# Performance work log

Hardware: AMD Instinct MI355X
Metric: run time of the kernel (lower is better)

## Reference

```python
import jax, jax.numpy as jnp
import numpy as np

B, F, H, W = 1, 4, 20, 44
P = H * W            # 880 tokens per frame (20*44, from max_attention_size = 15*880)
S = F * P            # 3520 packed tokens
DIM, NH, FFN, OUT = 1536, 12, 6144, 64   # OUT = prod(patch_size)*out_dim = 4*16
HD = DIM // NH       # 128
C = HD // 2          # 64 rotary complex pairs
EPS = 1e-6


def _rope_angles():
    # Wan 3D RoPE: split C pairs as (C-2*(C//3), C//3, C//3) over (frame, h, w)
    cf, ch, cw = C - 2 * (C // 3), C // 3, C // 3
    def tab(n, cp):
        inv = 1.0 / (10000.0 ** (np.arange(cp) / cp))
        return np.outer(np.arange(n), inv)
    af = np.broadcast_to(tab(F, cf)[:, None, None, :], (F, H, W, cf))
    ah = np.broadcast_to(tab(H, ch)[None, :, None, :], (F, H, W, ch))
    aw = np.broadcast_to(tab(W, cw)[None, None, :, :], (F, H, W, cw))
    return np.concatenate([af, ah, aw], -1).reshape(S, C).astype(np.float32)


def setup_inputs() -> dict:
    key = jax.random.key(0)
    ks = jax.random.split(key, 24)
    g = lambda i, shape, s=0.02: jax.random.normal(ks[i], shape, dtype=jnp.float32) * s
    inp = {
        'x': jax.random.normal(ks[0], (B, S, DIM), dtype=jnp.float32),
        'e': g(1, (B, F, 6, DIM), 1.0),
        'e_head': g(2, (B, F, 2, DIM), 1.0),
        'rope_angles': jnp.asarray(_rope_angles()),
        'mod_block': g(3, (1, 6, DIM), 1.0 / float(np.sqrt(DIM))),
        'mod_head': g(4, (1, 2, DIM), 1.0 / float(np.sqrt(DIM))),
        'Wq': g(5, (DIM, DIM)), 'bq': jnp.zeros((DIM,), jnp.float32),
        'Wk': g(6, (DIM, DIM)), 'bk': jnp.zeros((DIM,), jnp.float32),
        'Wv': g(7, (DIM, DIM)), 'bv': jnp.zeros((DIM,), jnp.float32),
        'Wo': g(8, (DIM, DIM)), 'bo': jnp.zeros((DIM,), jnp.float32),
        'wq_norm': jnp.ones((DIM,), jnp.float32),
        'wk_norm': jnp.ones((DIM,), jnp.float32),
        'W1': g(9, (DIM, FFN)), 'b1': jnp.zeros((FFN,), jnp.float32),
        'W2': g(10, (FFN, DIM)), 'b2': jnp.zeros((DIM,), jnp.float32),
        'Wh': g(11, (DIM, OUT)), 'bh': jnp.zeros((OUT,), jnp.float32),
    }
    return inp


def _ln(x):
    # WanLayerNorm without elementwise affine
    m = jnp.mean(x, axis=-1, keepdims=True)
    v = jnp.var(x, axis=-1, keepdims=True)
    return (x - m) * jax.lax.rsqrt(v + EPS)


def _rms(x, w):
    return x * jax.lax.rsqrt(jnp.mean(x * x, axis=-1, keepdims=True) + EPS) * w


def _rope(t, ang):
    # t: [B,S,NH,HD]; adjacent pairs form complex numbers (view_as_complex style)
    tr = t.reshape(B, S, NH, C, 2)
    cos = jnp.cos(ang)[None, :, None, :]
    sin = jnp.sin(ang)[None, :, None, :]
    t0, t1 = tr[..., 0], tr[..., 1]
    return jnp.stack([t0 * cos - t1 * sin, t0 * sin + t1 * cos], -1).reshape(B, S, NH, HD)


def reference(x, e, e_head, rope_angles, mod_block, mod_head,
              Wq, bq, Wk, bk, Wv, bv, Wo, bo, wq_norm, wk_norm,
              W1, b1, W2, b2, Wh, bh):
    # ---- AdaLN modulation split (6-way) ----
    em = mod_block[:, None] + e                      # [B,F,6,DIM]
    e0, e1, e2, e3, e4, e5 = [em[:, :, i][:, :, None, :] for i in range(6)]

    xf = x.reshape(B, F, P, DIM)
    h = (_ln(xf) * (1 + e1) + e0).reshape(B, S, DIM)

    # ---- QK-RMSNorm + RoPE self attention (block-causal, block = one frame) ----
    q = _rope(_rms(h @ Wq + bq, wq_norm).reshape(B, S, NH, HD), rope_angles)
    k = _rope(_rms(h @ Wk + bk, wk_norm).reshape(B, S, NH, HD), rope_angles)
    v = (h @ Wv + bv).reshape(B, S, NH, HD)

    blk = jnp.arange(S) // P
    mask = blk[None, :] <= blk[:, None]              # [S,S] block-causal
    scores = jnp.einsum('bqhd,bkhd->bhqk', q, k) / np.float32(np.sqrt(HD))
    scores = jnp.where(mask[None, None], scores, jnp.float32(-1e30))
    attn = jax.nn.softmax(scores, axis=-1)
    y = jnp.einsum('bhqk,bkhd->bqhd', attn, v).reshape(B, S, DIM) @ Wo + bo

    xf = xf + y.reshape(B, F, P, DIM) * e2

    # ---- FFN with AdaLN modulation ----
    hf = (_ln(xf) * (1 + e4) + e3).reshape(B, S, DIM)
    ff = jax.nn.gelu(hf @ W1 + b1) @ W2 + b2
    xf = xf + ff.reshape(B, F, P, DIM) * e5

    # ---- OutputHead: modulated norm + linear ----
    eh = mod_head[:, None] + e_head                  # [B,F,2,DIM]
    eh0 = eh[:, :, 0][:, :, None, :]
    eh1 = eh[:, :, 1][:, :, None, :]
    out = (_ln(xf) * (1 + eh1) + eh0) @ Wh + bh      # [B,F,P,OUT]
    return out
```

## Files before the change

### kernel.cpp

```cpp
#include <hip/hip_runtime.h>
#include <cstdint>
#include <cstddef>

typedef __bf16 bf16;
typedef __bf16 bf16x2 __attribute__((ext_vector_type(2)));
typedef __bf16 bf16x8 __attribute__((ext_vector_type(8)));
typedef float f32x4 __attribute__((ext_vector_type(4)));
typedef unsigned int u32x4 __attribute__((ext_vector_type(4)));

#define S_TOK 3520
#define S_PAD 3584
#define P_TOK 880
#define NFRM 4
#define DIM 1536
#define NH 12
#define HD 128
#define FFN_D 6144
#define NOUT 64
#define EPSV 1e-6f
#define QSCALE 0.12751743f

__device__ __forceinline__ f32x4 mfma16(bf16x8 a, bf16x8 b, f32x4 c) {
  return __builtin_amdgcn_mfma_f32_16x16x32_bf16(a, b, c, 0, 0, 0);
}

__device__ __forceinline__ void gload_lds16(const bf16* g, bf16* l) {
  __builtin_amdgcn_global_load_lds(
      (const __attribute__((address_space(1))) unsigned int*)g,
      (__attribute__((address_space(3))) unsigned int*)l, 16, 0, 0);
}

__device__ __forceinline__ uint32_t pk2(float lo, float hi) {
  bf16x2 t;
  t[0] = (bf16)lo;
  t[1] = (bf16)hi;
  return __builtin_bit_cast(uint32_t, t);
}

__global__ __launch_bounds__(256) void k_prep(const float* __restrict__ e,
                                              const float* __restrict__ e_head,
                                              const float* __restrict__ mod_block,
                                              const float* __restrict__ mod_head,
                                              float* __restrict__ em,
                                              float* __restrict__ ehm) {
  int i = blockIdx.x * 256 + threadIdx.x;
  if (i < NFRM * 6 * DIM) em[i] = mod_block[i % (6 * DIM)] + e[i];
  int j = i - NFRM * 6 * DIM;
  if (j >= 0 && j < NFRM * 2 * DIM) ehm[j] = mod_head[j % (2 * DIM)] + e_head[j];
}

__global__ __launch_bounds__(256) void k_zero_vpad(bf16* __restrict__ vc) {
  size_t base = ((size_t)blockIdx.x * 28 + 27) * 4096 + 2048 + (size_t)threadIdx.x * 8;
#pragma unroll
  for (int i = 0; i < 8; ++i) vc[base + i] = (bf16)0.f;
}

__global__ __launch_bounds__(256) void k_transpose(const float* __restrict__ W,
                                                   bf16* __restrict__ Wt, int K, int N) {
  __shared__ float tile[32][33];
  int n0 = blockIdx.x * 32, k0 = blockIdx.y * 32;
  int tx = threadIdx.x & 31, ty = threadIdx.x >> 5;
#pragma unroll
  for (int j = 0; j < 4; ++j) {
    int k = k0 + ty * 4 + j;
    float v = (n0 + tx < N) ? W[(size_t)k * N + n0 + tx] : 0.f;
    tile[ty * 4 + j][tx] = v;
  }
  __syncthreads();
#pragma unroll
  for (int j = 0; j < 4; ++j) {
    int n = n0 + ty * 4 + j;
    if (n < N) Wt[(size_t)n * K + k0 + tx] = (bf16)tile[tx][ty * 4 + j];
  }
}

__global__ __launch_bounds__(256) void k_adaln(const float* __restrict__ in,
                                               bf16* __restrict__ out,
                                               const float* __restrict__ e_shift,
                                               const float* __restrict__ e_scale,
                                               int fstride) {
  int tok = blockIdx.x;
  int t = threadIdx.x;
  bf16* orow = out + (size_t)tok * DIM;
  if (tok >= S_TOK) {
#pragma unroll
    for (int i = 0; i < 6; ++i) orow[t * 6 + i] = (bf16)0.f;
    return;
  }
  const float* xrow = in + (size_t)tok * DIM;
  float v[6];
  float s = 0.f, sq = 0.f;
#pragma unroll
  for (int i = 0; i < 6; ++i) {
    v[i] = xrow[t * 6 + i];
    s += v[i];
    sq += v[i] * v[i];
  }
  for (int off = 32; off; off >>= 1) {
    s += __shfl_down(s, off);
    sq += __shfl_down(sq, off);
  }
  __shared__ float red[8];
  int wv = t >> 6, lane = t & 63;
  if (lane == 0) { red[wv] = s; red[4 + wv] = sq; }
  __syncthreads();
  float ts = red[0] + red[1] + red[2] + red[3];
  float tq = red[4] + red[5] + red[6] + red[7];
  float mean = ts * (1.f / DIM);
  float var = tq * (1.f / DIM) - mean * mean;
  float rstd = rsqrtf(var + EPSV);
  int f = tok / P_TOK;
  const float* sh = e_shift + (size_t)f * fstride;
  const float* sc = e_scale + (size_t)f * fstride;
#pragma unroll
  for (int i = 0; i < 6; ++i) {
    int d = t * 6 + i;
    orow[d] = (bf16)((v[i] - mean) * rstd * (1.f + sc[d]) + sh[d]);
  }
}

__global__ __launch_bounds__(256) void k_qkv_post(const float* __restrict__ qkv,
                                                  const float* __restrict__ wqn,
                                                  const float* __restrict__ wkn,
                                                  const float* __restrict__ ang,
                                                  bf16* __restrict__ qb,
                                                  bf16* __restrict__ kb,
                                                  bf16* __restrict__ vc) {
  int s = blockIdx.x;
  int t = threadIdx.x;
  const float* row = qkv + (size_t)s * 3 * DIM;
  float qv[6], kv[6], vv[6];
  float sqq = 0.f, sqk = 0.f;
  int d0 = t * 6;
#pragma unroll
  for (int i = 0; i < 6; ++i) {
    int d = d0 + i;
    qv[i] = row[d];
    kv[i] = row[DIM + d];
    vv[i] = row[2 * DIM + d];
    sqq += qv[i] * qv[i];
    sqk += kv[i] * kv[i];
  }
  float a1 = sqq, a2 = sqk;
  for (int off = 32; off; off >>= 1) {
    a1 += __shfl_down(a1, off);
    a2 += __shfl_down(a2, off);
  }
  __shared__ float red[8];
  int wv = t >> 6, lane = t & 63;
  if (lane == 0) { red[wv] = a1; red[4 + wv] = a2; }
  __syncthreads();
  float tq = red[0] + red[1] + red[2] + red[3];
  float tk = red[4] + red[5] + red[6] + red[7];
  float rq = rsqrtf(tq * (1.f / DIM) + EPSV);
  float rk = rsqrtf(tk * (1.f / DIM) + EPSV);
#pragma unroll
  for (int p = 0; p < 3; ++p) {
    int d = d0 + p * 2;
    int h = d >> 7;
    int hd = d & 127;
    int c = hd >> 1;
    float a = ang[(size_t)s * 64 + c];
    float sa, ca;
    sincosf(a, &sa, &ca);
    float q0 = qv[p * 2] * rq * wqn[d], q1 = qv[p * 2 + 1] * rq * wqn[d + 1];
    float k0 = kv[p * 2] * rk * wkn[d], k1 = kv[p * 2 + 1] * rk * wkn[d + 1];
    size_t base = ((size_t)h * S_TOK + s) * HD + hd;
    qb[base]     = (bf16)((q0 * ca - q1 * sa) * QSCALE);
    qb[base + 1] = (bf16)((q0 * sa + q1 * ca) * QSCALE);
    kb[base]     = (bf16)(k0 * ca - k1 * sa);
    kb[base + 1] = (bf16)(k0 * sa + k1 * ca);
  }
  int f = s / P_TOK;
  int l = s - f * P_TOK;
  int lb = l >> 5, gg = (l >> 3) & 3, r = l & 7;
#pragma unroll
  for (int i = 0; i < 6; ++i) {
    int d = d0 + i;
    int h = d >> 7, hd = d & 127;
    vc[((((size_t)(h * NFRM + f)) * 28 + lb) * 512 + gg * 128 + hd) * 8 + r] = (bf16)vv[i];
  }
}

__global__ __launch_bounds__(320) void k_attn(const bf16* __restrict__ qb,
                                              const bf16* __restrict__ kb,
                                              const bf16* __restrict__ vc,
                                              float* __restrict__ parto,
                                              float* __restrict__ partml) {
  __shared__ __align__(16) bf16 Ks[2][512 * 8];
  __shared__ __align__(16) bf16 Vs[2][512 * 8];
  int h = blockIdx.x / 110;
  int p = blockIdx.x % 110;
  int f = (p < 11) ? 0 : (p < 33) ? 1 : (p < 66) ? 2 : 3;
  int cum = (f == 0) ? 0 : (f == 1) ? 11 : (f == 2) ? 33 : 66;
  int w = p - cum;
  int kc = w / 11;
  int qt = f * 11 + w % 11;
  int slot = blockIdx.x;
  int t = threadIdx.x;
  int wv = t >> 6, lane = t & 63;
  int r16 = lane & 15, g = lane >> 4;
  int q0 = qt * 80 + wv * 16;
  int kv0 = kc * P_TOK;
  const bf16* qbase = qb + ((size_t)h * S_TOK + q0 + r16) * HD + g * 8;
  bf16x8 qf[4];
#pragma unroll
  for (int kk = 0; kk < 4; ++kk) qf[kk] = *(const bf16x8*)(qbase + kk * 32);
  f32x4 acc[8] = {};
  float mrow = -1e30f, lrow = 0.f;
  int src01 = r16 + ((2 * g) & 3) * 16;
  int src23 = src01 + 16;
  bool glo = (g < 2);
  int sB = t + 256;
  int kr0 = t >> 4, kl0 = t & 15;
  int ks0 = (kl0 & 8) | ((kl0 ^ kr0) & 7);
  int kr1 = sB >> 4, kl1 = sB & 15;
  int ks1 = (kl1 & 8) | ((kl1 ^ kr1) & 7);
  const bf16* kh = kb + (size_t)h * S_TOK * HD;
  const bf16* vchunk = vc + ((size_t)(h * NFRM + kc)) * 28 * 4096;
#define STAGE_ATT(buf, jj)                                                  \
  do {                                                                      \
    int kvoj = (jj) * 32;                                                   \
    int gr0 = kv0 + kvoj + kr0; if (gr0 >= S_TOK) gr0 = 0;                  \
    int gr1 = kv0 + kvoj + kr1; if (gr1 >= S_TOK) gr1 = 0;                  \
    gload_lds16(kh + (size_t)gr0 * HD + ks0 * 8, Ks[buf] + t * 8);          \
    gload_lds16(kh + (size_t)gr1 * HD + ks1 * 8, Ks[buf] + sB * 8);         \
    gload_lds16(vchunk + (size_t)(jj) * 4096 + t * 8, Vs[buf] + t * 8);     \
    gload_lds16(vchunk + (size_t)(jj) * 4096 + sB * 8, Vs[buf] + sB * 8);   \
  } while (0)
  const int nsteps = (P_TOK + 31) >> 5;
  if (t < 256) STAGE_ATT(0, 0);
  int cur = 0;
  for (int j = 0; j < nsteps; ++j) {
    int kvo = j * 32;
    if (j + 1 < nsteps) {
      if (t < 256) STAGE_ATT(cur ^ 1, j + 1);
      asm volatile("s_waitcnt vmcnt(4)" ::: "memory");
    } else {
      asm volatile("s_waitcnt vmcnt(0)" ::: "memory");
    }
    __builtin_amdgcn_s_barrier();
    f32x4 st0 = {0.f, 0.f, 0.f, 0.f}, st1 = {0.f, 0.f, 0.f, 0.f};
#pragma unroll
    for (int kk = 0; kk < 4; ++kk) {
      int sl = g + 4 * kk;
      int ss = (sl & 8) | ((sl ^ r16) & 7);
      bf16x8 k0 = *(const bf16x8*)(Ks[cur] + (r16 * 16 + ss) * 8);
      bf16x8 k1 = *(const bf16x8*)(Ks[cur] + ((16 + r16) * 16 + ss) * 8);
      st0 = mfma16(k0, qf[kk], st0);
      st1 = mfma16(k1, qf[kk], st1);
    }
    float hm = (kvo + 16 >= P_TOK) ? -1e30f : 0.f;
    float a0[4], a1[4];
#pragma unroll
    for (int r = 0; r < 4; ++r) {
      a0[r] = st0[r];
      a1[r] = st1[r] + hm;
    }
    float tm = fmaxf(fmaxf(fmaxf(a0[0], a0[1]), fmaxf(a0[2], a0[3])),
                     fmaxf(fmaxf(a1[0], a1[1]), fmaxf(a1[2], a1[3])));
    tm = fmaxf(tm, __shfl_xor(tm, 16));
    tm = fmaxf(tm, __shfl_xor(tm, 32));
    float mn = fmaxf(mrow, tm);
    float p0[4], p1[4], ps = 0.f;
#pragma unroll
    for (int r = 0; r < 4; ++r) {
      p0[r] = exp2f(a0[r] - mn);
      p1[r] = exp2f(a1[r] - mn);
      ps += p0[r] + p1[r];
    }
    float scl = exp2f(mrow - mn);
    mrow = mn;
    lrow = lrow * scl + ps;
    uint32_t A0 = pk2(p0[0], p0[1]), A1 = pk2(p0[2], p0[3]);
    uint32_t B0 = pk2(p1[0], p1[1]), B1 = pk2(p1[2], p1[3]);
    uint32_t sA0 = __shfl(A0, src01), sA1 = __shfl(A1, src01);
    uint32_t sB0 = __shfl(B0, src01), sB1 = __shfl(B1, src01);
    uint32_t tA0 = __shfl(A0, src23), tA1 = __shfl(A1, src23);
    uint32_t tB0 = __shfl(B0, src23), tB1 = __shfl(B1, src23);
    u32x4 wds;
    wds[0] = glo ? sA0 : sB0;
    wds[1] = glo ? sA1 : sB1;
    wds[2] = glo ? tA0 : tB0;
    wds[3] = glo ? tA1 : tB1;
    bf16x8 pb = __builtin_bit_cast(bf16x8, wds);
#pragma unroll
    for (int hb = 0; hb < 8; ++hb) {
      acc[hb][0] *= scl;
      acc[hb][1] *= scl;
      acc[hb][2] *= scl;
      acc[hb][3] *= scl;
    }
    const bf16* vsl = Vs[cur] + (size_t)(g * 128 + r16) * 8;
#pragma unroll
    for (int hb = 0; hb < 8; ++hb) {
      bf16x8 vfr = *(const bf16x8*)(vsl + hb * 128);
      acc[hb] = mfma16(vfr, pb, acc[hb]);
    }
    asm volatile("" ::: "memory");
    __builtin_amdgcn_s_barrier();
    cur ^= 1;
  }
#undef STAGE_ATT
  lrow += __shfl_xor(lrow, 16);
  lrow += __shfl_xor(lrow, 32);
  float* obase = parto + (((size_t)slot * 5 + wv) * 8) * 256;
#pragma unroll
  for (int hb = 0; hb < 8; ++hb) {
    *(f32x4*)(obase + (hb * 64 + lane) * 4) = acc[hb];
  }
  if (g == 0) {
    float* mlb = partml + ((size_t)slot * 5 + wv) * 32;
    mlb[r16] = mrow;
    mlb[16 + r16] = lrow;
  }
}

__global__ __launch_bounds__(256) void k_att_reduce(const float* __restrict__ parto,
                                                    const float* __restrict__ partml,
                                                    bf16* __restrict__ attb) {
  int b = blockIdx.x;
  int h = b / 44, qt = b % 44;
  int f = qt / 11, j = qt % 11;
  int cum = (f == 0) ? 0 : (f == 1) ? 11 : (f == 2) ? 33 : 66;
  int t = threadIdx.x;
  int d = t & 127, half = t >> 7;
  int hb = d >> 4, g = (d >> 2) & 3, r = d & 3;
  int q0 = qt * 80;
  for (int it = 0; it < 40; ++it) {
    int qloc = it + 40 * half;
    int wv = qloc >> 4, r16 = qloc & 15;
    float m[4], l[4];
    float mt = -1e30f;
    for (int kc = 0; kc <= f; ++kc) {
      int slot = h * 110 + cum + kc * 11 + j;
      const float* mlb = partml + ((size_t)slot * 5 + wv) * 32;
      m[kc] = mlb[r16];
      l[kc] = mlb[16 + r16];
      mt = fmaxf(mt, m[kc]);
    }
    float lt = 0.f, o = 0.f;
    for (int kc = 0; kc <= f; ++kc) {
      int slot = h * 110 + cum + kc * 11 + j;
      float wgt = exp2f(m[kc] - mt);
      lt += l[kc] * wgt;
      o += parto[(((size_t)slot * 5 + wv) * 8 + hb) * 256 + (g * 16 + r16) * 4 + r] * wgt;
    }
    attb[(size_t)(q0 + qloc) * DIM + h * HD + d] = (bf16)(o / lt);
  }
}

struct GemmP {
  const bf16* A;
  const bf16* Bt;
  int K;
  int Mtiles;
  int Ntiles;
  int Mreal;
  int mode;
  const float* bias0;
  const float* bias1;
  const float* bias2;
  const float* res;
  const float* emod;
  int e_fstride;
  float* outf;
  bf16* outb;
  int ldo;
};

__global__ __launch_bounds__(512, 4) void k_gemm(GemmP p) {
  int nwg = p.Mtiles * p.Ntiles;
  int bid = blockIdx.x;
  int xq = nwg >> 3, xr = nwg & 7;
  int xcd = bid & 7, jj = bid >> 3;
  int wg = (xcd < xr ? xcd * (xq + 1) : xr * (xq + 1) + (xcd - xr) * xq) + jj;
  int bm = wg % p.Mtiles;
  int bn = wg / p.Mtiles;
  __shared__ __align__(16) bf16 Asl[2][128 * 64];
  __shared__ __align__(16) bf16 Bsl[2][128 * 64];
  int t = threadIdx.x, lane = t & 63, wv = t >> 6;
  int r16 = lane & 15, g = lane >> 4;
  int s7 = r16 & 7;
  int wr = wv >> 2, wc = wv & 3;
  f32x4 acc[4][2] = {};
  const bf16* Ag = p.A + (size_t)bm * 128 * p.K;
  const bf16* Bg = p.Bt + (size_t)bn * 128 * p.K;
  int b0 = t, b1 = t + 512;
  int rw0 = b0 >> 3, cb0 = (b0 & 7) ^ (rw0 & 7);
  int rw1 = b1 >> 3, cb1 = (b1 & 7) ^ (rw1 & 7);
#define STAGE(d, kt)                                                          \
  do {                                                                        \
    int k0s = (kt) * 64;                                                      \
    gload_lds16(Ag + (size_t)rw0 * p.K + k0s + cb0 * 8, Asl[d] + b0 * 8);     \
    gload_lds16(Ag + (size_t)rw1 * p.K + k0s + cb1 * 8, Asl[d] + b1 * 8);     \
    gload_lds16(Bg + (size_t)rw0 * p.K + k0s + cb0 * 8, Bsl[d] + b0 * 8);     \
    gload_lds16(Bg + (size_t)rw1 * p.K + k0s + cb1 * 8, Bsl[d] + b1 * 8);     \
  } while (0)
  const int nt = p.K >> 6;
  STAGE(0, 0);
  int cur = 0;
  for (int tt = 0; tt < nt; ++tt) {
    if (tt + 1 < nt) {
      STAGE(cur ^ 1, tt + 1);
      asm volatile("s_waitcnt vmcnt(4)" ::: "memory");
    } else {
      asm volatile("s_waitcnt vmcnt(0)" ::: "memory");
    }
    __builtin_amdgcn_s_barrier();
    bf16x8 af[4][2], bfr[2][2];
#pragma unroll
    for (int mi = 0; mi < 4; ++mi)
#pragma unroll
      for (int kk = 0; kk < 2; ++kk)
        af[mi][kk] = *(const bf16x8*)(Asl[cur] + (size_t)(wr * 64 + mi * 16 + r16) * 64 +
                                      (((kk * 4 + g) ^ s7) * 8));
#pragma unroll
    for (int ni = 0; ni < 2; ++ni)
#pragma unroll
      for (int kk = 0; kk < 2; ++kk)
        bfr[ni][kk] = *(const bf16x8*)(Bsl[cur] + (size_t)(wc * 32 + ni * 16 + r16) * 64 +
                                       (((kk * 4 + g) ^ s7) * 8));
    __builtin_amdgcn_s_setprio(1);
#pragma unroll
    for (int mi = 0; mi < 4; ++mi)
#pragma unroll
      for (int ni = 0; ni < 2; ++ni)
#pragma unroll
        for (int kk = 0; kk < 2; ++kk)
          acc[mi][ni] = mfma16(af[mi][kk], bfr[ni][kk], acc[mi][ni]);
    __builtin_amdgcn_s_setprio(0);
    asm volatile("" ::: "memory");
    __builtin_amdgcn_s_barrier();
    cur ^= 1;
  }
#undef STAGE
  int mbase = bm * 128 + wr * 64, nbase = bn * 128 + wc * 32;
#pragma unroll
  for (int mi = 0; mi < 4; ++mi) {
#pragma unroll
    for (int ni = 0; ni < 2; ++ni) {
      int col = nbase + ni * 16 + r16;
#pragma unroll
      for (int r = 0; r < 4; ++r) {
        int row = mbase + mi * 16 + 4 * g + r;
        if (row >= p.Mreal) continue;
        float v = acc[mi][ni][r];
        if (p.mode == 0) {
          float b = col < DIM ? p.bias0[col]
                              : (col < 2 * DIM ? p.bias1[col - DIM] : p.bias2[col - 2 * DIM]);
          p.outf[(size_t)row * p.ldo + col] = v + b;
        } else if (p.mode == 1) {
          int fr = row / P_TOK;
          p.outf[(size_t)row * p.ldo + col] =
              p.res[(size_t)row * DIM + col] +
              (v + p.bias0[col]) * p.emod[(size_t)fr * p.e_fstride + col];
        } else if (p.mode == 2) {
          float xg = v + p.bias0[col];
          float gl = 0.5f * xg * (1.f + tanhf(0.7978845608028654f * (xg + 0.044715f * xg * xg * xg)));
          p.outb[(size_t)row * p.ldo + col] = (bf16)gl;
        } else {
          if (col < NOUT) p.outf[(size_t)row * p.ldo + col] = v + p.bias0[col];
        }
      }
    }
  }
}

extern "C" void kernel_launch(void* const* d_in, const int* in_sizes, int n_in,
                              void* d_out, int out_size, void* d_ws, size_t ws_size,
                              hipStream_t stream) {
  const float* x = (const float*)d_in[0];
  const float* e = (const float*)d_in[1];
  const float* e_head = (const float*)d_in[2];
  const float* ang = (const float*)d_in[3];
  const float* mod_block = (const float*)d_in[4];
  const float* mod_head = (const float*)d_in[5];
  const float* Wq = (const float*)d_in[6];
  const float* bq = (const float*)d_in[7];
  const float* Wk = (const float*)d_in[8];
  const float* bk = (const float*)d_in[9];
  const float* Wv = (const float*)d_in[10];
  const float* bv = (const float*)d_in[11];
  const float* Wo = (const float*)d_in[12];
  const float* bo = (const float*)d_in[13];
  const float* wqn = (const float*)d_in[14];
  const float* wkn = (const float*)d_in[15];
  const float* W1 = (const float*)d_in[16];
  const float* b1 = (const float*)d_in[17];
  const float* W2 = (const float*)d_in[18];
  const float* b2 = (const float*)d_in[19];
  const float* Wh = (const float*)d_in[20];
  const float* bh = (const float*)d_in[21];
  float* out = (float*)d_out;
  char* ws = (char*)d_ws;

  size_t WT_QKV = 0;
  size_t WT_O = WT_QKV + (size_t)3 * DIM * DIM * 2;
  size_t W1T = WT_O + (size_t)DIM * DIM * 2;
  size_t W2T = W1T + (size_t)FFN_D * DIM * 2;
  size_t WHT = W2T + (size_t)DIM * FFN_D * 2;
  size_t EMOFF = WHT + (size_t)128 * DIM * 2;
  size_t EHOFF = EMOFF + (size_t)NFRM * 6 * DIM * 4;
  size_t HB = EHOFF + (size_t)NFRM * 2 * DIM * 4;
  size_t CQKV = HB + (size_t)S_PAD * DIM * 2;
  size_t DQB = CQKV + (size_t)S_TOK * 3 * DIM * 4;
  size_t EATT = DQB + (size_t)3 * NH * S_TOK * HD * 2;
  size_t GXF2 = EATT + (size_t)S_PAD * DIM * 2;
  size_t END = GXF2 + (size_t)S_TOK * DIM * 4;
  if (ws_size < END) return;

  bf16* wtqkv = (bf16*)(ws + WT_QKV);
  bf16* wto = (bf16*)(ws + WT_O);
  bf16* w1t = (bf16*)(ws + W1T);
  bf16* w2t = (bf16*)(ws + W2T);
  bf16* wht = (bf16*)(ws + WHT);
  float* em = (float*)(ws + EMOFF);
  float* ehm = (float*)(ws + EHOFF);
  bf16* hb = (bf16*)(ws + HB);
  float* qkvf = (float*)(ws + CQKV);
  bf16* ffb = (bf16*)(ws + CQKV);
  float* parto = (float*)(ws + CQKV);
  float* partml = parto + (size_t)1320 * 5 * 8 * 256;
  bf16* qbp = (bf16*)(ws + DQB);
  bf16* kbp = qbp + (size_t)NH * S_TOK * HD;
  bf16* vcp = kbp + (size_t)NH * S_TOK * HD;
  float* xf3 = (float*)(ws + DQB);
  bf16* attb = (bf16*)(ws + EATT);
  float* xf2 = (float*)(ws + GXF2);

  k_prep<<<(NFRM * 8 * DIM) / 256, 256, 0, stream>>>(e, e_head, mod_block, mod_head, em, ehm);
  k_zero_vpad<<<NH * NFRM, 256, 0, stream>>>(vcp);

  k_transpose<<<dim3(48, 48), 256, 0, stream>>>(Wq, wtqkv, DIM, DIM);
  k_transpose<<<dim3(48, 48), 256, 0, stream>>>(Wk, wtqkv + (size_t)DIM * DIM, DIM, DIM);
  k_transpose<<<dim3(48, 48), 256, 0, stream>>>(Wv, wtqkv + (size_t)2 * DIM * DIM, DIM, DIM);
  k_transpose<<<dim3(48, 48), 256, 0, stream>>>(Wo, wto, DIM, DIM);
  k_transpose<<<dim3(192, 48), 256, 0, stream>>>(W1, w1t, DIM, FFN_D);
  k_transpose<<<dim3(48, 192), 256, 0, stream>>>(W2, w2t, FFN_D, DIM);
  k_transpose<<<dim3(2, 48), 256, 0, stream>>>(Wh, wht, DIM, NOUT);
  hipMemsetAsync(ws + WHT + (size_t)NOUT * DIM * 2, 0, (size_t)(128 - NOUT) * DIM * 2, stream);
  hipMemsetAsync(ws + EATT + (size_t)S_TOK * DIM * 2, 0, (size_t)(S_PAD - S_TOK) * DIM * 2, stream);

  k_adaln<<<S_PAD, 256, 0, stream>>>(x, hb, em, em + DIM, 6 * DIM);

  GemmP g0{};
  g0.A = hb; g0.Bt = wtqkv; g0.K = DIM; g0.Mtiles = 28; g0.Ntiles = 36; g0.Mreal = S_TOK;
  g0.mode = 0; g0.bias0 = bq; g0.bias1 = bk; g0.bias2 = bv; g0.outf = qkvf; g0.ldo = 3 * DIM;
  k_gemm<<<28 * 36, 512, 0, stream>>>(g0);

  k_qkv_post<<<S_TOK, 256, 0, stream>>>(qkvf, wqn, wkn, ang, qbp, kbp, vcp);

  k_attn<<<NH * 110, 320, 0, stream>>>(qbp, kbp, vcp, parto, partml);
  k_att_reduce<<<NH * 44, 256, 0, stream>>>(parto, partml, attb);

  GemmP g1{};
  g1.A = attb; g1.Bt = wto; g1.K = DIM; g1.Mtiles = 28; g1.Ntiles = 12; g1.Mreal = S_TOK;
  g1.mode = 1; g1.bias0 = bo; g1.res = x; g1.emod = em + 2 * DIM; g1.e_fstride = 6 * DIM;
  g1.outf = xf2; g1.ldo = DIM;
  k_gemm<<<28 * 12, 512, 0, stream>>>(g1);

  k_adaln<<<S_PAD, 256, 0, stream>>>(xf2, hb, em + 3 * DIM, em + 4 * DIM, 6 * DIM);

  GemmP g2{};
  g2.A = hb; g2.Bt = w1t; g2.K = DIM; g2.Mtiles = 28; g2.Ntiles = 48; g2.Mreal = S_TOK;
  g2.mode = 2; g2.bias0 = b1; g2.outb = ffb; g2.ldo = FFN_D;
  k_gemm<<<28 * 48, 512, 0, stream>>>(g2);
  hipMemsetAsync(ws + CQKV + (size_t)S_TOK * FFN_D * 2, 0, (size_t)(S_PAD - S_TOK) * FFN_D * 2, stream);

  GemmP g3{};
  g3.A = ffb; g3.Bt = w2t; g3.K = FFN_D; g3.Mtiles = 28; g3.Ntiles = 12; g3.Mreal = S_TOK;
  g3.mode = 1; g3.bias0 = b2; g3.res = xf2; g3.emod = em + 5 * DIM; g3.e_fstride = 6 * DIM;
  g3.outf = xf3; g3.ldo = DIM;
  k_gemm<<<28 * 12, 512, 0, stream>>>(g3);

  k_adaln<<<S_PAD, 256, 0, stream>>>(xf3, hb, ehm, ehm + DIM, 2 * DIM);

  GemmP g4{};
  g4.A = hb; g4.Bt = wht; g4.K = DIM; g4.Mtiles = 28; g4.Ntiles = 1; g4.Mreal = S_TOK;
  g4.mode = 4; g4.bias0 = bh; g4.outf = out; g4.ldo = NOUT;
  k_gemm<<<28, 512, 0, stream>>>(g4);
}
```

Baseline: 689.7 us.

## Store QKV in bf16, swizzle V LDS layout, defer softmax rescaling

The QKV GEMM now writes bf16 instead of fp32, which halves the intermediate traffic read by the QK-norm/RoPE kernel. The attention kernel XOR-swizzles how V is staged into LDS to reduce bank conflicts on the V fragment reads. It also skips the online-softmax accumulator rescale whenever no row max grows by more than a threshold, as in FA-style lazy rescaling. The costs are an extra bf16 rounding of QKV before RMSNorm, and exponents up to 2^8 under the stale max, which widens the bf16 range of P.

```diff
diff --git a/kernel.cpp b/kernel.cpp
--- a/kernel.cpp
+++ b/kernel.cpp
@@ -119,7 +119,7 @@
   }
 }
 
-__global__ __launch_bounds__(256) void k_qkv_post(const float* __restrict__ qkv,
+__global__ __launch_bounds__(256) void k_qkv_post(const bf16* __restrict__ qkv,
                                                   const float* __restrict__ wqn,
                                                   const float* __restrict__ wkn,
                                                   const float* __restrict__ ang,
@@ -128,16 +128,16 @@
                                                   bf16* __restrict__ vc) {
   int s = blockIdx.x;
   int t = threadIdx.x;
-  const float* row = qkv + (size_t)s * 3 * DIM;
+  const bf16* row = qkv + (size_t)s * 3 * DIM;
   float qv[6], kv[6], vv[6];
   float sqq = 0.f, sqk = 0.f;
   int d0 = t * 6;
 #pragma unroll
   for (int i = 0; i < 6; ++i) {
     int d = d0 + i;
-    qv[i] = row[d];
-    kv[i] = row[DIM + d];
-    vv[i] = row[2 * DIM + d];
+    qv[i] = (float)row[d];
+    kv[i] = (float)row[DIM + d];
+    vv[i] = (float)row[2 * DIM + d];
     sqq += qv[i] * qv[i];
     sqk += kv[i] * kv[i];
   }
@@ -216,6 +216,8 @@
   int ks0 = (kl0 & 8) | ((kl0 ^ kr0) & 7);
   int kr1 = sB >> 4, kl1 = sB & 15;
   int ks1 = (kl1 & 8) | ((kl1 ^ kr1) & 7);
+  int vu0 = t ^ (((t >> 7) & 3) << 1);
+  int vu1 = sB ^ (((sB >> 7) & 3) << 1);
   const bf16* kh = kb + (size_t)h * S_TOK * HD;
   const bf16* vchunk = vc + ((size_t)(h * NFRM + kc)) * 28 * 4096;
 #define STAGE_ATT(buf, jj)                                                  \
@@ -225,14 +227,14 @@
     int gr1 = kv0 + kvoj + kr1; if (gr1 >= S_TOK) gr1 = 0;                  \
     gload_lds16(kh + (size_t)gr0 * HD + ks0 * 8, Ks[buf] + t * 8);          \
     gload_lds16(kh + (size_t)gr1 * HD + ks1 * 8, Ks[buf] + sB * 8);         \
-    gload_lds16(vchunk + (size_t)(jj) * 4096 + t * 8, Vs[buf] + t * 8);     \
-    gload_lds16(vchunk + (size_t)(jj) * 4096 + sB * 8, Vs[buf] + sB * 8);   \
+    gload_lds16(vchunk + (size_t)(jj) * 4096 + vu0 * 8, Vs[buf] + t * 8);   \
+    gload_lds16(vchunk + (size_t)(jj) * 4096 + vu1 * 8, Vs[buf] + sB * 8);  \
   } while (0)
   const int nsteps = (P_TOK + 31) >> 5;
   if (t < 256) STAGE_ATT(0, 0);
   int cur = 0;
+  int vrb = g * 128 + (r16 ^ ((g & 3) << 1));
   for (int j = 0; j < nsteps; ++j) {
-    int kvo = j * 32;
     if (j + 1 < nsteps) {
       if (t < 256) STAGE_ATT(cur ^ 1, j + 1);
       asm volatile("s_waitcnt vmcnt(4)" ::: "memory");
@@ -250,7 +252,7 @@
       st0 = mfma16(k0, qf[kk], st0);
       st1 = mfma16(k1, qf[kk], st1);
     }
-    float hm = (kvo + 16 >= P_TOK) ? -1e30f : 0.f;
+    float hm = (j == nsteps - 1) ? -1e30f : 0.f;
     float a0[4], a1[4];
 #pragma unroll
     for (int r = 0; r < 4; ++r) {
@@ -261,17 +263,28 @@
                      fmaxf(fmaxf(a1[0], a1[1]), fmaxf(a1[2], a1[3])));
     tm = fmaxf(tm, __shfl_xor(tm, 16));
     tm = fmaxf(tm, __shfl_xor(tm, 32));
-    float mn = fmaxf(mrow, tm);
+    bool defer = __all(tm <= mrow + 8.f);
+    if (!defer) {
+      float mn = fmaxf(mrow, tm);
+      float scl = exp2f(mrow - mn);
+      lrow *= scl;
+#pragma unroll
+      for (int hb = 0; hb < 8; ++hb) {
+        acc[hb][0] *= scl;
+        acc[hb][1] *= scl;
+        acc[hb][2] *= scl;
+        acc[hb][3] *= scl;
+      }
+      mrow = mn;
+    }
     float p0[4], p1[4], ps = 0.f;
 #pragma unroll
     for (int r = 0; r < 4; ++r) {
-      p0[r] = exp2f(a0[r] - mn);
-      p1[r] = exp2f(a1[r] - mn);
+      p0[r] = exp2f(a0[r] - mrow);
+      p1[r] = exp2f(a1[r] - mrow);
       ps += p0[r] + p1[r];
     }
-    float scl = exp2f(mrow - mn);
-    mrow = mn;
-    lrow = lrow * scl + ps;
+    lrow += ps;
     uint32_t A0 = pk2(p0[0], p0[1]), A1 = pk2(p0[2], p0[3]);
     uint32_t B0 = pk2(p1[0], p1[1]), B1 = pk2(p1[2], p1[3]);
     uint32_t sA0 = __shfl(A0, src01), sA1 = __shfl(A1, src01);
@@ -284,14 +297,7 @@
     wds[2] = glo ? tA0 : tB0;
     wds[3] = glo ? tA1 : tB1;
     bf16x8 pb = __builtin_bit_cast(bf16x8, wds);
-#pragma unroll
-    for (int hb = 0; hb < 8; ++hb) {
-      acc[hb][0] *= scl;
-      acc[hb][1] *= scl;
-      acc[hb][2] *= scl;
-      acc[hb][3] *= scl;
-    }
-    const bf16* vsl = Vs[cur] + (size_t)(g * 128 + r16) * 8;
+    const bf16* vsl = Vs[cur] + (size_t)vrb * 8;
 #pragma unroll
     for (int hb = 0; hb < 8; ++hb) {
       bf16x8 vfr = *(const bf16x8*)(vsl + hb * 128);
@@ -449,7 +455,7 @@
         if (p.mode == 0) {
           float b = col < DIM ? p.bias0[col]
                               : (col < 2 * DIM ? p.bias1[col - DIM] : p.bias2[col - 2 * DIM]);
-          p.outf[(size_t)row * p.ldo + col] = v + b;
+          p.outb[(size_t)row * p.ldo + col] = (bf16)(v + b);
         } else if (p.mode == 1) {
           int fr = row / P_TOK;
           p.outf[(size_t)row * p.ldo + col] =
@@ -518,7 +524,7 @@
   float* em = (float*)(ws + EMOFF);
   float* ehm = (float*)(ws + EHOFF);
   bf16* hb = (bf16*)(ws + HB);
-  float* qkvf = (float*)(ws + CQKV);
+  bf16* qkvb = (bf16*)(ws + CQKV);
   bf16* ffb = (bf16*)(ws + CQKV);
   float* parto = (float*)(ws + CQKV);
   float* partml = parto + (size_t)1320 * 5 * 8 * 256;
@@ -546,10 +552,10 @@
 
   GemmP g0{};
   g0.A = hb; g0.Bt = wtqkv; g0.K = DIM; g0.Mtiles = 28; g0.Ntiles = 36; g0.Mreal = S_TOK;
-  g0.mode = 0; g0.bias0 = bq; g0.bias1 = bk; g0.bias2 = bv; g0.outf = qkvf; g0.ldo = 3 * DIM;
+  g0.mode = 0; g0.bias0 = bq; g0.bias1 = bk; g0.bias2 = bv; g0.outb = qkvb; g0.ldo = 3 * DIM;
   k_gemm<<<28 * 36, 512, 0, stream>>>(g0);
 
-  k_qkv_post<<<S_TOK, 256, 0, stream>>>(qkvf, wqn, wkn, ang, qbp, kbp, vcp);
+  k_qkv_post<<<S_TOK, 256, 0, stream>>>(qkvb, wqn, wkn, ang, qbp, kbp, vcp);
 
   k_attn<<<NH * 110, 320, 0, stream>>>(qbp, kbp, vcp, parto, partml);
   k_att_reduce<<<NH * 44, 256, 0, stream>>>(parto, partml, attb);
```

New measurement: 661.4 us. 1.04x faster.
